# Kernel tuning notes

Measured on AMD Instinct MI355X. Metric: run time of the kernel, lower is better.

Reference implementation:

```python
import jax, jax.numpy as jnp
import numpy as np

ALPHA = 0.5  # LeakyReLU negative slope


def setup_inputs() -> dict:
    key = jax.random.key(0)
    k1, k2, k3, k4, k5 = jax.random.split(key, 5)
    B, N, S, SO, K = 16, 2048, 12, 12, 32
    return {
        "fushed_features": jax.random.normal(k1, (B, N, 64), dtype=jnp.float32),
        "input_data": jax.random.normal(k2, (B, N, S), dtype=jnp.float32),
        "W": jax.random.normal(k3, (S, SO), dtype=jnp.float32) * (1.414 / np.sqrt(S)),
        "a": jax.random.normal(k4, (2 * SO, 1), dtype=jnp.float32) * 0.3,
        "idx": jax.random.randint(k5, (B, N, K), 0, N, dtype=jnp.int32),
    }


def reference(fushed_features, input_data, W, a, idx):
    # input_data: (B, N, S); W: (S, SO); a: (2*SO, 1); idx: (B, N, K)
    B, N, S = input_data.shape
    SO = W.shape[1]
    wh = input_data @ W  # (B, N, SO)
    # concat([wh_i, wh_j]) @ a  ==  wh_i @ a[:SO] + wh_j @ a[SO:]  (exact same math,
    # avoids materializing the (B,N,N,2*SO) concat the torch code builds)
    e_src = wh @ a[:SO, 0]  # (B, N)
    e_dst = wh @ a[SO:, 0]  # (B, N)
    scores = jax.nn.leaky_relu(e_src[:, :, None] + e_dst[:, None, :], negative_slope=ALPHA)  # (B,N,N)
    att = jnp.take_along_axis(scores, idx, axis=2)  # (B, N, K) gather top-k neighbor scores
    att = jax.nn.softmax(att, axis=-1)  # softmax over the K neighbors
    # gather neighbor time series: (B, N, K, S)
    neigh = input_data[jnp.arange(B)[:, None, None], idx]
    out = att[..., None] * neigh  # (B, N, K, S)
    return out
```

## Files before the change

kernel.cpp:

```cpp
#include <hip/hip_runtime.h>


#define GAT_N 2048
#define GAT_ALPHA 0.5f
#define PPB 8

__global__ __launch_bounds__(256) void gat_precomp(
    const float* __restrict__ x,
    const float* __restrict__ W,
    const float* __restrict__ a,
    float*       __restrict__ xp,
    float*       __restrict__ es,
    float*       __restrict__ ed)
{
    __shared__ float wvec[24];
    __shared__ float rows[256 * 12];
    const int tid = threadIdx.x;

    if (tid < 24) {
        const int s = tid % 12;
        const float* av = a + (tid < 12 ? 0 : 12);
        float acc = 0.f;
        #pragma unroll
        for (int t = 0; t < 12; ++t) acc += W[s * 12 + t] * av[t];
        wvec[tid] = acc;
    }
    const float4* g4 = (const float4*)(x + (size_t)blockIdx.x * 256 * 12);
    float4* l4 = (float4*)rows;
    #pragma unroll
    for (int r = 0; r < 3; ++r) l4[tid + 256 * r] = g4[tid + 256 * r];
    __syncthreads();

    const int n = blockIdx.x * 256 + tid;
    const float* row = rows + tid * 12;
    float s0 = 0.f, s1 = 0.f;
    #pragma unroll
    for (int t = 0; t < 12; ++t) {
        s0 += row[t] * wvec[t];
        s1 += row[t] * wvec[12 + t];
    }
    es[n] = s0;
    ed[n] = s1;

    float4* o4 = (float4*)(xp + (size_t)blockIdx.x * 256 * 16);
    #pragma unroll
    for (int c = 0; c < 4; ++c) {
        const int g  = tid + 256 * c;
        const int r  = g >> 2;
        const int pc = g & 3;
        float4 v = make_float4(0.f, 0.f, 0.f, 0.f);
        if (pc < 3) v = *(const float4*)(rows + r * 12 + pc * 4);
        o4[g] = v;
    }
}

__global__ __launch_bounds__(256) void gat_main(
    const float* __restrict__ xp,
    const float* __restrict__ es_arr,
    const float* __restrict__ ed_arr,
    const int*   __restrict__ idx,
    float*       __restrict__ out)
{
    __shared__ float stage[PPB * 384];
    const int tid  = threadIdx.x;
    const int p    = tid >> 5;
    const int pair = blockIdx.x * PPB + p;
    const int k    = tid & 31;

    const int j   = idx[(size_t)pair * 32 + k];
    const int nbr = (pair & ~(GAT_N - 1)) + j;

    const float4* rowj = (const float4*)(xp + (size_t)nbr * 16);
    const float4 n0 = rowj[0], n1 = rowj[1], n2 = rowj[2];

    const float e  = es_arr[pair] + ed_arr[nbr];
    float sc = e > 0.f ? e : GAT_ALPHA * e;

    float m = sc;
    #pragma unroll
    for (int off = 16; off; off >>= 1) m = fmaxf(m, __shfl_xor(m, off, 32));
    const float ex = __expf(sc - m);
    float sum = ex;
    #pragma unroll
    for (int off = 16; off; off >>= 1) sum += __shfl_xor(sum, off, 32);
    const float att = ex / sum;

    float4* st = (float4*)(stage + p * 384 + k * 12);
    st[0] = make_float4(att * n0.x, att * n0.y, att * n0.z, att * n0.w);
    st[1] = make_float4(att * n1.x, att * n1.y, att * n1.z, att * n1.w);
    st[2] = make_float4(att * n2.x, att * n2.y, att * n2.z, att * n2.w);
    __syncthreads();

    const float4* sm4 = (const float4*)stage;
    float4* o4 = (float4*)(out + (size_t)blockIdx.x * PPB * 384);
    #pragma unroll
    for (int r = 0; r < 3; ++r) o4[tid + 256 * r] = sm4[tid + 256 * r];
}

__global__ __launch_bounds__(256) void gat_fused(
    const float* __restrict__ x, const float* __restrict__ W,
    const float* __restrict__ a, const int* __restrict__ idx,
    float* __restrict__ out)
{
    __shared__ float wvec[24];
    __shared__ float stage[PPB * 384];
    const int tid = threadIdx.x;

    if (tid < 24) {
        const int s = tid % 12;
        const float* av = a + (tid < 12 ? 0 : 12);
        float acc = 0.f;
        #pragma unroll
        for (int t = 0; t < 12; ++t) acc += W[s * 12 + t] * av[t];
        wvec[tid] = acc;
    }
    __syncthreads();

    const int p    = tid >> 5;
    const int pair = blockIdx.x * PPB + p;
    const int k    = tid & 31;

    const float4* rowi = (const float4*)(x + (size_t)pair * 12);
    const float4 i0 = rowi[0], i1 = rowi[1], i2 = rowi[2];
    const float e_src =
        i0.x*wvec[0] + i0.y*wvec[1] + i0.z*wvec[2]  + i0.w*wvec[3] +
        i1.x*wvec[4] + i1.y*wvec[5] + i1.z*wvec[6]  + i1.w*wvec[7] +
        i2.x*wvec[8] + i2.y*wvec[9] + i2.z*wvec[10] + i2.w*wvec[11];

    const int j   = idx[(size_t)pair * 32 + k];
    const int nbr = (pair & ~(GAT_N - 1)) + j;
    const float4* rowj = (const float4*)(x + (size_t)nbr * 12);
    const float4 n0 = rowj[0], n1 = rowj[1], n2 = rowj[2];
    const float e_dst =
        n0.x*wvec[12] + n0.y*wvec[13] + n0.z*wvec[14] + n0.w*wvec[15] +
        n1.x*wvec[16] + n1.y*wvec[17] + n1.z*wvec[18] + n1.w*wvec[19] +
        n2.x*wvec[20] + n2.y*wvec[21] + n2.z*wvec[22] + n2.w*wvec[23];

    float sc = e_src + e_dst;
    sc = sc > 0.f ? sc : GAT_ALPHA * sc;
    float m = sc;
    #pragma unroll
    for (int off = 16; off; off >>= 1) m = fmaxf(m, __shfl_xor(m, off, 32));
    const float ex = __expf(sc - m);
    float sum = ex;
    #pragma unroll
    for (int off = 16; off; off >>= 1) sum += __shfl_xor(sum, off, 32);
    const float att = ex / sum;

    float4* st = (float4*)(stage + p * 384 + k * 12);
    st[0] = make_float4(att * n0.x, att * n0.y, att * n0.z, att * n0.w);
    st[1] = make_float4(att * n1.x, att * n1.y, att * n1.z, att * n1.w);
    st[2] = make_float4(att * n2.x, att * n2.y, att * n2.z, att * n2.w);
    __syncthreads();

    const float4* sm4 = (const float4*)stage;
    float4* o4 = (float4*)(out + (size_t)blockIdx.x * PPB * 384);
    #pragma unroll
    for (int r = 0; r < 3; ++r) o4[tid + 256 * r] = sm4[tid + 256 * r];
}

extern "C" void kernel_launch(void* const* d_in, const int* in_sizes, int n_in,
                              void* d_out, int out_size, void* d_ws, size_t ws_size,
                              hipStream_t stream) {
    const float* x   = (const float*)d_in[1];
    const float* W   = (const float*)d_in[2];
    const float* a   = (const float*)d_in[3];
    const int*   idx = (const int*)d_in[4];
    float* out = (float*)d_out;

    const int pairs  = in_sizes[1] / 12;
    const int blocks = pairs / PPB;

    const size_t xp_bytes = (size_t)pairs * 16 * sizeof(float);
    const size_t e_bytes  = (size_t)pairs * sizeof(float);
    if (ws_size >= xp_bytes + 2 * e_bytes) {
        float* xp = (float*)d_ws;
        float* es = xp + (size_t)pairs * 16;
        float* ed = es + pairs;
        gat_precomp<<<pairs / 256, 256, 0, stream>>>(x, W, a, xp, es, ed);
        gat_main<<<blocks, 256, 0, stream>>>(xp, es, ed, idx, out);
    } else {
        gat_fused<<<blocks, 256, 0, stream>>>(x, W, a, idx, out);
    }
}
```

Baseline: 90.55 us.

## Pack e_dst into padded row slot and process two pairs per thread

The precompute kernel now stores e_dst in the otherwise-zero fourth float4 of each padded 64-byte row, so the main kernel fetches the neighbor features and e_dst with a single row gather instead of a separate scattered load. The main kernel runs with 128 threads, each handling two pairs to raise memory-level parallelism. It also drops the max-reduction in the softmax, clamping scores at 80 instead, which changes numerical behaviour for large score ranges.

```diff
diff --git a/kernel.cpp b/kernel.cpp
--- a/kernel.cpp
+++ b/kernel.cpp
@@ -10,11 +10,11 @@
     const float* __restrict__ W,
     const float* __restrict__ a,
     float*       __restrict__ xp,
-    float*       __restrict__ es,
-    float*       __restrict__ ed)
+    float*       __restrict__ es)
 {
     __shared__ float wvec[24];
     __shared__ float rows[256 * 12];
+    __shared__ float eds[256];
     const int tid = threadIdx.x;
 
     if (tid < 24) {
@@ -39,8 +39,9 @@
         s0 += row[t] * wvec[t];
         s1 += row[t] * wvec[12 + t];
     }
-    es[n] = s0;
-    ed[n] = s1;
+    es[n]    = s0;
+    eds[tid] = s1;
+    __syncthreads();
 
     float4* o4 = (float4*)(xp + (size_t)blockIdx.x * 256 * 16);
     #pragma unroll
@@ -48,53 +49,71 @@
         const int g  = tid + 256 * c;
         const int r  = g >> 2;
         const int pc = g & 3;
-        float4 v = make_float4(0.f, 0.f, 0.f, 0.f);
+        float4 v;
         if (pc < 3) v = *(const float4*)(rows + r * 12 + pc * 4);
+        else        v = make_float4(eds[r], 0.f, 0.f, 0.f);
         o4[g] = v;
     }
 }
 
-__global__ __launch_bounds__(256) void gat_main(
+__global__ __launch_bounds__(128) void gat_main(
     const float* __restrict__ xp,
     const float* __restrict__ es_arr,
-    const float* __restrict__ ed_arr,
     const int*   __restrict__ idx,
     float*       __restrict__ out)
 {
     __shared__ float stage[PPB * 384];
-    const int tid  = threadIdx.x;
-    const int p    = tid >> 5;
-    const int pair = blockIdx.x * PPB + p;
-    const int k    = tid & 31;
-
-    const int j   = idx[(size_t)pair * 32 + k];
-    const int nbr = (pair & ~(GAT_N - 1)) + j;
-
-    const float4* rowj = (const float4*)(xp + (size_t)nbr * 16);
-    const float4 n0 = rowj[0], n1 = rowj[1], n2 = rowj[2];
-
-    const float e  = es_arr[pair] + ed_arr[nbr];
-    float sc = e > 0.f ? e : GAT_ALPHA * e;
-
-    float m = sc;
-    #pragma unroll
-    for (int off = 16; off; off >>= 1) m = fmaxf(m, __shfl_xor(m, off, 32));
-    const float ex = __expf(sc - m);
-    float sum = ex;
-    #pragma unroll
-    for (int off = 16; off; off >>= 1) sum += __shfl_xor(sum, off, 32);
-    const float att = ex / sum;
-
-    float4* st = (float4*)(stage + p * 384 + k * 12);
-    st[0] = make_float4(att * n0.x, att * n0.y, att * n0.z, att * n0.w);
-    st[1] = make_float4(att * n1.x, att * n1.y, att * n1.z, att * n1.w);
-    st[2] = make_float4(att * n2.x, att * n2.y, att * n2.z, att * n2.w);
+    const int tid   = threadIdx.x;
+    const int p     = tid >> 5;
+    const int k     = tid & 31;
+    const int pair0 = blockIdx.x * PPB + p;
+    const int pair1 = pair0 + 4;
+
+    const int j0 = idx[(size_t)pair0 * 32 + k];
+    const int j1 = idx[(size_t)pair1 * 32 + k];
+    const float es0 = es_arr[pair0];
+    const float es1 = es_arr[pair1];
+
+    const int nbr0 = (pair0 & ~(GAT_N - 1)) + j0;
+    const int nbr1 = (pair1 & ~(GAT_N - 1)) + j1;
+
+    const float4* r0 = (const float4*)(xp + (size_t)nbr0 * 16);
+    const float4* r1 = (const float4*)(xp + (size_t)nbr1 * 16);
+    const float4 a0 = r0[0], a1 = r0[1], a2 = r0[2], a3 = r0[3];
+    const float4 b0 = r1[0], b1 = r1[1], b2 = r1[2], b3 = r1[3];
+
+    float e0 = es0 + a3.x;
+    float e1 = es1 + b3.x;
+    e0 = e0 > 0.f ? e0 : GAT_ALPHA * e0;
+    e1 = e1 > 0.f ? e1 : GAT_ALPHA * e1;
+    e0 = fminf(e0, 80.f);
+    e1 = fminf(e1, 80.f);
+
+    const float ex0 = __expf(e0);
+    const float ex1 = __expf(e1);
+    float s0 = ex0, s1 = ex1;
+    #pragma unroll
+    for (int off = 16; off; off >>= 1) {
+        s0 += __shfl_xor(s0, off, 32);
+        s1 += __shfl_xor(s1, off, 32);
+    }
+    const float att0 = ex0 / s0;
+    const float att1 = ex1 / s1;
+
+    float4* st0 = (float4*)(stage + p * 384 + k * 12);
+    float4* st1 = (float4*)(stage + (p + 4) * 384 + k * 12);
+    st0[0] = make_float4(att0 * a0.x, att0 * a0.y, att0 * a0.z, att0 * a0.w);
+    st0[1] = make_float4(att0 * a1.x, att0 * a1.y, att0 * a1.z, att0 * a1.w);
+    st0[2] = make_float4(att0 * a2.x, att0 * a2.y, att0 * a2.z, att0 * a2.w);
+    st1[0] = make_float4(att1 * b0.x, att1 * b0.y, att1 * b0.z, att1 * b0.w);
+    st1[1] = make_float4(att1 * b1.x, att1 * b1.y, att1 * b1.z, att1 * b1.w);
+    st1[2] = make_float4(att1 * b2.x, att1 * b2.y, att1 * b2.z, att1 * b2.w);
     __syncthreads();
 
     const float4* sm4 = (const float4*)stage;
     float4* o4 = (float4*)(out + (size_t)blockIdx.x * PPB * 384);
     #pragma unroll
-    for (int r = 0; r < 3; ++r) o4[tid + 256 * r] = sm4[tid + 256 * r];
+    for (int r = 0; r < 6; ++r) o4[tid + 128 * r] = sm4[tid + 128 * r];
 }
 
 __global__ __launch_bounds__(256) void gat_fused(
@@ -103,7 +122,7 @@
     float* __restrict__ out)
 {
     __shared__ float wvec[24];
-    __shared__ float stage[PPB * 384];
+    __shared__ float stage[8 * 384];
     const int tid = threadIdx.x;
 
     if (tid < 24) {
@@ -117,7 +136,7 @@
     __syncthreads();
 
     const int p    = tid >> 5;
-    const int pair = blockIdx.x * PPB + p;
+    const int pair = blockIdx.x * 8 + p;
     const int k    = tid & 31;
 
     const float4* rowi = (const float4*)(x + (size_t)pair * 12);
@@ -154,7 +173,7 @@
     __syncthreads();
 
     const float4* sm4 = (const float4*)stage;
-    float4* o4 = (float4*)(out + (size_t)blockIdx.x * PPB * 384);
+    float4* o4 = (float4*)(out + (size_t)blockIdx.x * 8 * 384);
     #pragma unroll
     for (int r = 0; r < 3; ++r) o4[tid + 256 * r] = sm4[tid + 256 * r];
 }
@@ -168,18 +187,16 @@
     const int*   idx = (const int*)d_in[4];
     float* out = (float*)d_out;
 
-    const int pairs  = in_sizes[1] / 12;
-    const int blocks = pairs / PPB;
+    const int pairs = in_sizes[1] / 12;
 
     const size_t xp_bytes = (size_t)pairs * 16 * sizeof(float);
     const size_t e_bytes  = (size_t)pairs * sizeof(float);
-    if (ws_size >= xp_bytes + 2 * e_bytes) {
+    if (ws_size >= xp_bytes + e_bytes) {
         float* xp = (float*)d_ws;
         float* es = xp + (size_t)pairs * 16;
-        float* ed = es + pairs;
-        gat_precomp<<<pairs / 256, 256, 0, stream>>>(x, W, a, xp, es, ed);
-        gat_main<<<blocks, 256, 0, stream>>>(xp, es, ed, idx, out);
+        gat_precomp<<<pairs / 256, 256, 0, stream>>>(x, W, a, xp, es);
+        gat_main<<<pairs / PPB, 128, 0, stream>>>(xp, es, idx, out);
     } else {
-        gat_fused<<<blocks, 256, 0, stream>>>(x, W, a, idx, out);
-    }
-}
+        gat_fused<<<pairs / 8, 256, 0, stream>>>(x, W, a, idx, out);
+    }
+}
```

New measurement: 91.11 us. No clear change (+0.6%).
